# Optimization experiments

Measured on AMD Instinct MI355X. Metric: run time of the kernel, lower is better.

The kernel has to match this reference:

```python
import jax, jax.numpy as jnp
import numpy as np

B, T, E, H = 4, 2048, 1024, 2048  # note: T must equal H (mask shape constraint in source)


def setup_inputs() -> dict:
    key = jax.random.key(0)
    ks = jax.random.split(key, 5)
    x = jax.random.normal(ks[0], (B, T, E), dtype=jnp.float32)
    Wq = jax.random.normal(ks[1], (E, H), dtype=jnp.float32) * 0.02
    bq = jnp.zeros((H,), dtype=jnp.float32)
    Wv = jax.random.normal(ks[2], (E, H), dtype=jnp.float32) * 0.02
    bv = jnp.zeros((H,), dtype=jnp.float32)
    return {"x": x, "Wq": Wq, "bq": bq, "Wv": Wv, "bv": bv}


def reference(x, Wq, bq, Wv, bv):
    # NOTE: original code uses q_proj for BOTH q and k (k = self.q_proj(x)),
    # so k is identical to q; k_proj params are dead. We reproduce that.
    q = x @ Wq + bq                                  # [B, T, H]
    v = x @ Wv + bv                                  # [B, T, H]
    scores = jnp.einsum('bqd,bkd->bqk', q, q)        # q @ k.mT with k == q
    scaled = scores / jnp.sqrt(jnp.float32(Wq.shape[1]))
    mask = jnp.tril(jnp.ones((scaled.shape[1], scaled.shape[2]), dtype=scaled.dtype))
    masked = scaled * mask                           # multiplicative mask (as in source)
    attn = jax.nn.softmax(masked, axis=1)            # softmax over dim=1 (query axis), as in source
    return attn @ v                                  # [B, T, H]
```

## Files before the change

kernel.cpp:

```cpp
#include <hip/hip_runtime.h>


#define B_DIM 4
#define T_DIM 2048
#define E_DIM 1024
#define H_DIM 2048

typedef __attribute__((ext_vector_type(8))) short bf16x8;
typedef __attribute__((ext_vector_type(4))) short s16x4;
typedef __attribute__((ext_vector_type(4))) float f32x4;

__device__ __forceinline__ float bf2f(short s) {
  union { float f; unsigned u; } x; x.u = ((unsigned)(unsigned short)s) << 16; return x.f;
}
__device__ __forceinline__ short f2bf(float f) {
  union { float f; unsigned u; } x; x.f = f;
  unsigned r = x.u + 0x7fff + ((x.u >> 16) & 1);
  return (short)(r >> 16);
}

__device__ __forceinline__ void gload16(const short* g, short* l) {
  __builtin_amdgcn_global_load_lds(
      (const __attribute__((address_space(1))) void*)g,
      (__attribute__((address_space(3))) void*)l, 16, 0, 0);
}

template<int MODE>
__global__ __launch_bounds__(256) void gemm_bt(
    const short* __restrict__ Ag, const short* __restrict__ Bg,
    const float* __restrict__ bias, const float* __restrict__ bias2,
    void* __restrict__ Cg, void* __restrict__ Cg2,
    float* __restrict__ colsum, const float* __restrict__ sfx,
    int M, int N, int K, long sA, long sB, long sC, float scale)
{
  __shared__ __align__(16) short lds[128 * 64 * 2];
  short* As = lds;
  short* Bs = lds + 128 * 64;
  __shared__ float csum[128];

  const int t = threadIdx.x;
  const int bz = blockIdx.z;

  int rt, ct;
  if (MODE == 1) {
    int idx = 135 - blockIdx.x;
    rt = (int)((sqrtf(8.0f * idx + 1.0f) - 1.0f) * 0.5f);
    while ((rt + 1) * (rt + 2) / 2 <= idx) rt++;
    while (rt * (rt + 1) / 2 > idx) rt--;
    ct = idx - rt * (rt + 1) / 2;
  } else if (MODE == 2) {
    rt = (gridDim.x - 1) - blockIdx.x;
    ct = blockIdx.y;
  } else {
    rt = blockIdx.y; ct = blockIdx.x;
  }

  const short* A = Ag + (long)bz * sA + (long)rt * 128 * K;
  const short* B = Bg + (long)bz * sB + (long)ct * 128 * K;
  const int kEnd = (MODE == 2) ? (rt + 1) * 128 : K;

  const int lane = t & 63;
  const int wave = t >> 6;
  const int wr = wave >> 1, wc = wave & 1;
  const int l16 = lane & 15, kg = lane >> 4;

  if (MODE == 1) { if (t < 128) csum[t] = (rt == ct) ? 128.0f * ct : 0.0f; }

  f32x4 acc[4][4] = {};

  for (int k0 = 0; k0 < kEnd; k0 += 64) {
    __syncthreads();
#pragma unroll
    for (int j = 0; j < 4; ++j) {
      const int e = j * 256 + t;
      const int r = e >> 3, cl = e & 7;
      const int cg = cl ^ (r & 7);
      gload16(A + (long)r * K + (k0 + cg * 8), &As[e * 8]);
      gload16(B + (long)r * K + (k0 + cg * 8), &Bs[e * 8]);
    }
    __syncthreads();
#pragma unroll
    for (int kk = 0; kk < 2; ++kk) {
      bf16x8 af[4], bfr[4];
#pragma unroll
      for (int mi = 0; mi < 4; ++mi)
        af[mi] = *(const bf16x8*)&As[(wr * 64 + mi * 16 + l16) * 64 +
                                     ((kk * 4 + kg) ^ (l16 & 7)) * 8];
#pragma unroll
      for (int ni = 0; ni < 4; ++ni)
        bfr[ni] = *(const bf16x8*)&Bs[(wc * 64 + ni * 16 + l16) * 64 +
                                      ((kk * 4 + kg) ^ (l16 & 7)) * 8];
#pragma unroll
      for (int mi = 0; mi < 4; ++mi)
#pragma unroll
        for (int ni = 0; ni < 4; ++ni)
          acc[mi][ni] = __builtin_amdgcn_mfma_f32_16x16x32_bf16(af[mi], bfr[ni], acc[mi][ni], 0, 0, 0);
    }
  }

  if (MODE == 1) {
    short* Cs = lds;
    __syncthreads();
    float ps[4] = {0.f, 0.f, 0.f, 0.f};
#pragma unroll
    for (int mi = 0; mi < 4; ++mi)
#pragma unroll
      for (int ni = 0; ni < 4; ++ni) {
        const int cl = wc * 64 + ni * 16 + l16;
        const int col = ct * 128 + cl;
#pragma unroll
        for (int r = 0; r < 4; ++r) {
          const int rl = wr * 64 + kg * 4 + mi * 16 + r;
          const int row = rt * 128 + rl;
          float e = (row >= col) ? __expf(acc[mi][ni][r] * scale) : 1.0f;
          Cs[rl * 128 + cl] = f2bf(e);
          ps[ni] += e;
        }
      }
#pragma unroll
    for (int ni = 0; ni < 4; ++ni)
      atomicAdd(&csum[wc * 64 + ni * 16 + l16], ps[ni]);
    __syncthreads();
    short* C = (short*)Cg + (long)bz * sC;
    const int rr = t >> 1, cc = (t & 1) * 64;
    const long gbase = (long)(rt * 128 + rr) * N + ct * 128 + cc;
#pragma unroll
    for (int j = 0; j < 8; ++j)
      *(bf16x8*)(C + gbase + j * 8) = *(const bf16x8*)&Cs[rr * 128 + cc + j * 8];
    if (t < 128)
      atomicAdd(&colsum[(long)bz * N + ct * 128 + t], csum[t]);
  } else if (MODE == 0) {
    short* Cs = lds;
    __syncthreads();
    const int Nh = N >> 1;
#pragma unroll
    for (int mi = 0; mi < 4; ++mi)
#pragma unroll
      for (int ni = 0; ni < 4; ++ni) {
        const int cl = wc * 64 + ni * 16 + l16;
        const int colg = ct * 128 + cl;
        const float bv = (colg < Nh) ? bias[colg] : bias2[colg - Nh];
#pragma unroll
        for (int r = 0; r < 4; ++r) {
          const int rl = wr * 64 + kg * 4 + mi * 16 + r;
          Cs[rl * 128 + cl] = f2bf(acc[mi][ni][r] + bv);
        }
      }
    __syncthreads();
    short* C = (ct * 128 < Nh) ? (short*)Cg : (short*)Cg2;
    const int colofs = (ct * 128) & (Nh - 1);
    const int rr = t >> 1, cc = (t & 1) * 64;
    const long gbase = (long)(rt * 128 + rr) * Nh + colofs + cc;
#pragma unroll
    for (int j = 0; j < 8; ++j)
      *(bf16x8*)(C + gbase + j * 8) = *(const bf16x8*)&Cs[rr * 128 + cc + j * 8];
  } else {
    const int rowb = rt * 128 + wr * 64 + kg * 4;
    const int colb = ct * 128 + wc * 64 + l16;
    float* C = (float*)Cg + (long)bz * sC;
    const float* sf = sfx + ((long)bz * 16 + rt) * N;
#pragma unroll
    for (int mi = 0; mi < 4; ++mi)
#pragma unroll
      for (int ni = 0; ni < 4; ++ni) {
        int col = colb + ni * 16;
        float s = sf[col];
#pragma unroll
        for (int r = 0; r < 4; ++r) {
          int row = rowb + mi * 16 + r;
          C[(long)row * N + col] = acc[mi][ni][r] + s;
        }
      }
  }
}

__global__ __launch_bounds__(256) void f32_to_bf16(
    const float* __restrict__ src, short* __restrict__ dst, long n)
{
  long i = ((long)blockIdx.x * blockDim.x + threadIdx.x) * 4;
  if (i < n) {
    const float4 v = *(const float4*)(src + i);
    s16x4 o;
    o.x = f2bf(v.x); o.y = f2bf(v.y); o.z = f2bf(v.z); o.w = f2bf(v.w);
    *(s16x4*)(dst + i) = o;
  }
}

__global__ __launch_bounds__(256) void wtrans(
    const float* __restrict__ src0, const float* __restrict__ src1,
    short* __restrict__ dst)
{
  __shared__ short tile[64][65];
  const int t = threadIdx.x;
  const int c0 = blockIdx.x * 64;
  const int r0 = blockIdx.y * 64;
  const float* s = blockIdx.z ? src1 : src0;
  short* d = dst + (long)blockIdx.z * H_DIM * E_DIM;
  const int rl = t >> 4, cb = (t & 15) * 4;
#pragma unroll
  for (int i = 0; i < 4; ++i) {
    int r = rl + i * 16;
    const float4 w = *(const float4*)(s + (long)(r0 + r) * H_DIM + c0 + cb);
    tile[r][cb + 0] = f2bf(w.x); tile[r][cb + 1] = f2bf(w.y);
    tile[r][cb + 2] = f2bf(w.z); tile[r][cb + 3] = f2bf(w.w);
  }
  __syncthreads();
#pragma unroll
  for (int i = 0; i < 4; ++i) {
    int rr = rl + i * 16;
    s16x4 o;
    o.x = tile[cb + 0][rr]; o.y = tile[cb + 1][rr];
    o.z = tile[cb + 2][rr]; o.w = tile[cb + 3][rr];
    *(s16x4*)(d + (long)(c0 + rr) * E_DIM + r0 + cb) = o;
  }
}

__global__ __launch_bounds__(256) void vtrans(
    const short* __restrict__ src, short* __restrict__ dst,
    const float* __restrict__ sums)
{
  __shared__ short tile[64][65];
  const int t = threadIdx.x;
  const int c0 = blockIdx.x * 64;
  const int r0 = blockIdx.y * 64;
  const int bz = blockIdx.z;
  const short* s = src + (long)bz * T_DIM * H_DIM;
  short* d = dst + (long)bz * H_DIM * T_DIM;
  const float* su = sums + (long)bz * T_DIM;
  const int rl = t >> 4, cb = (t & 15) * 4;
#pragma unroll
  for (int i = 0; i < 4; ++i) {
    int r = rl + i * 16;
    const float rs = 1.0f / su[r0 + r];
    const s16x4 w = *(const s16x4*)(s + (long)(r0 + r) * H_DIM + c0 + cb);
    tile[r][cb + 0] = f2bf(bf2f(w.x) * rs); tile[r][cb + 1] = f2bf(bf2f(w.y) * rs);
    tile[r][cb + 2] = f2bf(bf2f(w.z) * rs); tile[r][cb + 3] = f2bf(bf2f(w.w) * rs);
  }
  __syncthreads();
#pragma unroll
  for (int i = 0; i < 4; ++i) {
    int rr = rl + i * 16;
    s16x4 o;
    o.x = tile[cb + 0][rr]; o.y = tile[cb + 1][rr];
    o.z = tile[cb + 2][rr]; o.w = tile[cb + 3][rr];
    *(s16x4*)(d + (long)(c0 + rr) * T_DIM + r0 + cb) = o;
  }
}

__global__ __launch_bounds__(256) void block_psum(
    const short* __restrict__ v, const float* __restrict__ colsum,
    float* __restrict__ psum)
{
  const int h = (blockIdx.x * 256 + threadIdx.x) * 2;
  const int j = blockIdx.y, bz = blockIdx.z;
  const short* vb = v + (long)bz * T_DIM * H_DIM;
  const float* cs = colsum + (long)bz * T_DIM;
  float s0 = 0.f, s1 = 0.f;
  const int k0 = j * 128;
  for (int k = k0; k < k0 + 128; ++k) {
    union { int i; short s[2]; } w;
    w.i = *(const int*)(vb + (long)k * H_DIM + h);
    const float rs = 1.0f / cs[k];
    s0 += bf2f(w.s[0]) * rs;
    s1 += bf2f(w.s[1]) * rs;
  }
  float* p = psum + ((long)bz * 16 + j) * H_DIM + h;
  p[0] = s0; p[1] = s1;
}

__global__ __launch_bounds__(256) void suffix_scan(
    const float* __restrict__ psum, float* __restrict__ sfx)
{
  const int h = blockIdx.x * 256 + threadIdx.x;
  const int bz = blockIdx.z;
  const long base = (long)bz * 16 * H_DIM + h;
  float suf = 0.f;
  sfx[base + 15L * H_DIM] = 0.f;
  for (int j = 15; j >= 1; --j) {
    suf += psum[base + (long)j * H_DIM];
    sfx[base + (long)(j - 1) * H_DIM] = suf;
  }
}

extern "C" void kernel_launch(void* const* d_in, const int* in_sizes, int n_in,
                              void* d_out, int out_size, void* d_ws, size_t ws_size,
                              hipStream_t stream) {
  const float* x  = (const float*)d_in[0];
  const float* Wq = (const float*)d_in[1];
  const float* bq = (const float*)d_in[2];
  const float* Wv = (const float*)d_in[3];
  const float* bv = (const float*)d_in[4];
  float* out = (float*)d_out;

  char* ws = (char*)d_ws;
  short* P      = (short*)(ws);
  short* q      = (short*)(ws + (size_t)32 * 1024 * 1024);
  short* v      = (short*)(ws + (size_t)64 * 1024 * 1024);
  float* colsum = (float*)(ws + (size_t)96 * 1024 * 1024);
  float* sfx    = (float*)(ws + (size_t)96 * 1024 * 1024 + 32 * 1024);
  short* vT = q;

  short* xb    = (short*)d_out;
  short* WqvT  = (short*)((char*)d_out + (size_t)16 * 1024 * 1024);
  float* psum  = (float*)((char*)d_out + (size_t)24 * 1024 * 1024);

  const float scale = 0.022097086912079612f;
  dim3 blk(256);

  hipMemsetAsync(colsum, 0, (size_t)B_DIM * T_DIM * 4, stream);

  f32_to_bf16<<<dim3((B_DIM * T_DIM * E_DIM) / (256 * 4)), blk, 0, stream>>>(
      x, xb, (long)B_DIM * T_DIM * E_DIM);
  wtrans<<<dim3(H_DIM / 64, E_DIM / 64, 2), blk, 0, stream>>>(Wq, Wv, WqvT);

  gemm_bt<0><<<dim3((2 * H_DIM) / 128, (B_DIM * T_DIM) / 128, 1), blk, 0, stream>>>(
      xb, WqvT, bq, bv, q, v, nullptr, nullptr,
      B_DIM * T_DIM, 2 * H_DIM, E_DIM, 0, 0, 0, 1.f);

  gemm_bt<1><<<dim3(136, 1, B_DIM), blk, 0, stream>>>(
      q, q, nullptr, nullptr, P, nullptr, colsum, nullptr, T_DIM, T_DIM, H_DIM,
      (long)T_DIM * H_DIM, (long)T_DIM * H_DIM, (long)T_DIM * T_DIM, scale);

  vtrans<<<dim3(H_DIM / 64, T_DIM / 64, B_DIM), blk, 0, stream>>>(v, vT, colsum);
  block_psum<<<dim3(H_DIM / 512, 16, B_DIM), blk, 0, stream>>>(v, colsum, psum);
  suffix_scan<<<dim3(H_DIM / 256, 1, B_DIM), blk, 0, stream>>>(psum, sfx);

  gemm_bt<2><<<dim3(T_DIM / 128, H_DIM / 128, B_DIM), blk, 0, stream>>>(
      P, vT, nullptr, nullptr, out, nullptr, nullptr, sfx, T_DIM, H_DIM, T_DIM,
      (long)T_DIM * T_DIM, (long)H_DIM * T_DIM, (long)T_DIM * H_DIM, 1.f);
}
```

Measured before the change: 370.0 us.

## Add 256x256-tile 512-thread GEMM with 4-stage LDS pipeline for projection and PV

Measured after the change: 359.3 us. -2.9%, faster.

```diff
diff --git a/kernel.cpp b/kernel.cpp
--- a/kernel.cpp
+++ b/kernel.cpp
@@ -23,6 +23,146 @@
   __builtin_amdgcn_global_load_lds(
       (const __attribute__((address_space(1))) void*)g,
       (__attribute__((address_space(3))) void*)l, 16, 0, 0);
+}
+
+template<int MODE>
+__global__ __launch_bounds__(512, 2) void gemm256(
+    const short* __restrict__ Ag, const short* __restrict__ Bg,
+    const float* __restrict__ bias, const float* __restrict__ bias2,
+    void* __restrict__ Cg, void* __restrict__ Cg2,
+    const float* __restrict__ sfx,
+    int N, int K, long sA, long sB, long sC)
+{
+  __shared__ __align__(16) short lds[4 * 16384];
+
+  const int t = threadIdx.x;
+  const int lane = t & 63, wave = t >> 6;
+  const int wm = wave >> 2, wn = wave & 3;
+  const int l16 = lane & 15, kg = lane >> 4;
+
+  int rt, ct, bz;
+  if (MODE == 2) { rt = blockIdx.x; ct = blockIdx.y; bz = blockIdx.z; }
+  else           { rt = blockIdx.y; ct = blockIdx.x; bz = 0; }
+
+  const short* A  = Ag + (long)bz * sA + (long)rt * 256 * K;
+  const short* Bp = Bg + (long)bz * sB + (long)ct * 256 * K;
+  const int kEnd = (MODE == 2) ? (rt + 1) * 256 : K;
+  const int NT = kEnd >> 5;
+
+  const int sr = t >> 2;
+  const int scg = (t & 3) ^ ((sr >> 2) & 3);
+  const long a0 = (long)sr * K + scg * 8;
+  const long a1 = a0 + 128L * K;
+
+  const int swz = kg ^ ((l16 >> 2) & 3);
+  const int aoff = (wm * 128 + l16) * 32 + swz * 8;
+  const int boff = (wn * 64 + l16) * 32 + swz * 8;
+
+  f32x4 acc[8][4] = {};
+
+#pragma unroll
+  for (int s = 0; s < 3; ++s) {
+    short* L = &lds[s * 16384];
+    const long k0 = (long)s * 32;
+    gload16(A + a0 + k0, L + t * 8);
+    gload16(A + a1 + k0, L + 4096 + t * 8);
+    gload16(Bp + a0 + k0, L + 8192 + t * 8);
+    gload16(Bp + a1 + k0, L + 12288 + t * 8);
+  }
+  asm volatile("s_waitcnt vmcnt(8)" ::: "memory");
+  __builtin_amdgcn_s_barrier();
+
+  for (int ts = 0; ts < NT; ++ts) {
+    const short* Ab = &lds[(ts & 3) * 16384];
+    const short* Bb = Ab + 8192;
+    short* Ls = &lds[((ts + 3) & 3) * 16384];
+    const long k3 = (long)(ts + 3) * 32;
+    const bool st = (ts + 3) < NT;
+
+    bf16x8 bfrag[4], afrag[4];
+#pragma unroll
+    for (int n = 0; n < 4; ++n) bfrag[n] = *(const bf16x8*)&Bb[boff + n * 512];
+#pragma unroll
+    for (int m = 0; m < 4; ++m) afrag[m] = *(const bf16x8*)&Ab[aoff + m * 512];
+    if (st) {
+      gload16(A + a0 + k3, Ls + t * 8);
+      gload16(A + a1 + k3, Ls + 4096 + t * 8);
+    }
+    __builtin_amdgcn_s_barrier();
+    __builtin_amdgcn_s_setprio(1);
+#pragma unroll
+    for (int m = 0; m < 4; ++m)
+#pragma unroll
+      for (int n = 0; n < 4; ++n)
+        acc[m][n] = __builtin_amdgcn_mfma_f32_16x16x32_bf16(afrag[m], bfrag[n], acc[m][n], 0, 0, 0);
+    __builtin_amdgcn_s_setprio(0);
+    __builtin_amdgcn_s_barrier();
+#pragma unroll
+    for (int m = 0; m < 4; ++m) afrag[m] = *(const bf16x8*)&Ab[aoff + (m + 4) * 512];
+    if (st) {
+      gload16(Bp + a0 + k3, Ls + 8192 + t * 8);
+      gload16(Bp + a1 + k3, Ls + 12288 + t * 8);
+    }
+    __builtin_amdgcn_s_barrier();
+    __builtin_amdgcn_s_setprio(1);
+#pragma unroll
+    for (int m = 0; m < 4; ++m)
+#pragma unroll
+      for (int n = 0; n < 4; ++n)
+        acc[m + 4][n] = __builtin_amdgcn_mfma_f32_16x16x32_bf16(afrag[m], bfrag[n], acc[m + 4][n], 0, 0, 0);
+    __builtin_amdgcn_s_setprio(0);
+    asm volatile("s_waitcnt lgkmcnt(0)" ::: "memory");
+    const int w = NT - 2 - ts;
+    if (w >= 2)      asm volatile("s_waitcnt vmcnt(8)" ::: "memory");
+    else if (w == 1) asm volatile("s_waitcnt vmcnt(4)" ::: "memory");
+    else if (w == 0) asm volatile("s_waitcnt vmcnt(0)" ::: "memory");
+    __builtin_amdgcn_s_barrier();
+  }
+
+  __syncthreads();
+
+  if (MODE == 0) {
+    short* Cs = lds;
+    const int Nh = N >> 1;
+#pragma unroll
+    for (int m = 0; m < 8; ++m)
+#pragma unroll
+      for (int n = 0; n < 4; ++n) {
+        const int cl = wn * 64 + n * 16 + l16;
+        const int colg = ct * 256 + cl;
+        const float bv = (colg < Nh) ? bias[colg] : bias2[colg - Nh];
+#pragma unroll
+        for (int r = 0; r < 4; ++r) {
+          const int rl = wm * 128 + m * 16 + kg * 4 + r;
+          *(short*)((char*)Cs + (((((rl << 8) + cl) << 1)) ^ ((rl & 7) << 4))) =
+              f2bf(acc[m][n][r] + bv);
+        }
+      }
+    __syncthreads();
+    short* C = ((ct * 256) < Nh) ? (short*)Cg : (short*)Cg2;
+    const int rr = t >> 1, hc = (t & 1) * 128;
+    const long gbase = (long)(rt * 256 + rr) * Nh + ((ct * 256) & (Nh - 1)) + hc;
+#pragma unroll
+    for (int j = 0; j < 16; ++j)
+      *(bf16x8*)(C + gbase + j * 8) =
+          *(const bf16x8*)((const char*)Cs +
+              ((((rr << 8) + hc + (j << 3)) << 1) ^ ((rr & 7) << 4)));
+  } else {
+    float* C = (float*)Cg + (long)bz * sC;
+    const float* sf = sfx + ((long)bz * 16 + 2 * rt + 1) * N;
+    const int rowb = rt * 256 + wm * 128 + kg * 4;
+    const int colb = ct * 256 + wn * 64 + l16;
+#pragma unroll
+    for (int m = 0; m < 8; ++m)
+#pragma unroll
+      for (int n = 0; n < 4; ++n) {
+        const int col = colb + n * 16;
+        const float s = sf[col];
+#pragma unroll
+        for (int r = 0; r < 4; ++r)
+          C[(long)(rowb + m * 16 + r) * N + col] = acc[m][n][r] + s;
+      }
+  }
 }
 
 template<int MODE>
@@ -174,6 +314,21 @@
   }
 }
 
+__global__ __launch_bounds__(256) void ones_fill(short* __restrict__ P)
+{
+  const int r = blockIdx.x, bz = blockIdx.z;
+  short* p = P + (long)bz * T_DIM * T_DIM +
+             (long)(2 * r) * 128 * T_DIM + (2 * r + 1) * 128;
+  const int t = threadIdx.x;
+  const int row = t >> 1, c0 = (t & 1) * 64;
+  bf16x8 ones;
+#pragma unroll
+  for (int j = 0; j < 8; ++j) ones[j] = (short)0x3F80;
+#pragma unroll
+  for (int j = 0; j < 8; ++j)
+    *(bf16x8*)(p + (long)row * T_DIM + c0 + j * 8) = ones;
+}
+
 __global__ __launch_bounds__(256) void f32_to_bf16(
     const float* __restrict__ src, short* __restrict__ dst, long n)
 {
@@ -313,19 +468,20 @@
       x, xb, (long)B_DIM * T_DIM * E_DIM);
   wtrans<<<dim3(H_DIM / 64, E_DIM / 64, 2), blk, 0, stream>>>(Wq, Wv, WqvT);
 
-  gemm_bt<0><<<dim3((2 * H_DIM) / 128, (B_DIM * T_DIM) / 128, 1), blk, 0, stream>>>(
-      xb, WqvT, bq, bv, q, v, nullptr, nullptr,
-      B_DIM * T_DIM, 2 * H_DIM, E_DIM, 0, 0, 0, 1.f);
+  gemm256<0><<<dim3((2 * H_DIM) / 256, (B_DIM * T_DIM) / 256, 1), dim3(512), 0, stream>>>(
+      xb, WqvT, bq, bv, q, v, nullptr, 2 * H_DIM, E_DIM, 0, 0, 0);
 
   gemm_bt<1><<<dim3(136, 1, B_DIM), blk, 0, stream>>>(
       q, q, nullptr, nullptr, P, nullptr, colsum, nullptr, T_DIM, T_DIM, H_DIM,
       (long)T_DIM * H_DIM, (long)T_DIM * H_DIM, (long)T_DIM * T_DIM, scale);
 
+  ones_fill<<<dim3(8, 1, B_DIM), blk, 0, stream>>>(P);
+
   vtrans<<<dim3(H_DIM / 64, T_DIM / 64, B_DIM), blk, 0, stream>>>(v, vT, colsum);
   block_psum<<<dim3(H_DIM / 512, 16, B_DIM), blk, 0, stream>>>(v, colsum, psum);
   suffix_scan<<<dim3(H_DIM / 256, 1, B_DIM), blk, 0, stream>>>(psum, sfx);
 
-  gemm_bt<2><<<dim3(T_DIM / 128, H_DIM / 128, B_DIM), blk, 0, stream>>>(
-      P, vT, nullptr, nullptr, out, nullptr, nullptr, sfx, T_DIM, H_DIM, T_DIM,
-      (long)T_DIM * T_DIM, (long)H_DIM * T_DIM, (long)T_DIM * H_DIM, 1.f);
-}
+  gemm256<2><<<dim3(T_DIM / 256, H_DIM / 256, B_DIM), dim3(512), 0, stream>>>(
+      P, vT, nullptr, nullptr, out, nullptr, sfx, H_DIM, T_DIM,
+      (long)T_DIM * T_DIM, (long)H_DIM * T_DIM, (long)T_DIM * H_DIM);
+}
```
